# Performance work log

Measured on AMD Instinct MI355X. Metric: run time of the kernel, lower is better.

## Reference

```python
import jax, jax.numpy as jnp
import numpy as np
import math

NB_STEPS = 50  # matches init kwarg nb_steps


def cc_quadrature(nb_steps):
    # Clenshaw-Curtis weights/nodes, identical to UMNN's compute_cc_weights.
    lam = np.arange(nb_steps + 1, dtype=np.float64).reshape(-1, 1)
    lam = np.cos((lam @ lam.T) * math.pi / nb_steps)
    lam[:, 0] = 0.5
    lam[:, -1] = 0.5 * lam[:, -1]
    lam = lam * 2.0 / nb_steps
    W = np.arange(nb_steps + 1, dtype=np.float64).reshape(-1, 1)
    W[np.arange(1, nb_steps + 1, 2)] = 0
    W = 2.0 / (1.0 - W ** 2)
    W[0] = 1
    W[np.arange(1, nb_steps + 1, 2)] = 0
    cc_weights = (lam.T @ W).astype(np.float32)                 # [K, 1]
    steps = np.cos(np.arange(nb_steps + 1, dtype=np.float64).reshape(-1, 1)
                   * math.pi / nb_steps).astype(np.float32)     # [K, 1]
    return jnp.asarray(cc_weights), jnp.asarray(steps)


def integrand_mlp(xh, W1, b1, W2, b2, W3, b3, W4, b4):
    y = jax.nn.relu(jnp.einsum('bkd,hd->bkh', xh, W1) + b1)
    y = jax.nn.relu(jnp.einsum('bkh,gh->bkg', y, W2) + b2)
    y = jax.nn.relu(jnp.einsum('bkg,fg->bkf', y, W3) + b3)
    y = jnp.einsum('bkf,of->bko', y, W4) + b4
    return jax.nn.elu(y) + 1.0


def setup_inputs() -> dict:
    key = jax.random.key(0)
    ks = jax.random.split(key, 10)
    B, HD, IN_D = 16384, 128, 64
    x = jax.random.normal(ks[0], (B, 1), dtype=jnp.float32)
    h = jax.random.normal(ks[1], (B, IN_D - 1), dtype=jnp.float32)
    def lin(k, fan_out, fan_in):
        return jax.random.normal(k, (fan_out, fan_in), dtype=jnp.float32) / np.sqrt(fan_in)
    return {
        'x': x, 'h': h,
        'W1': lin(ks[2], HD, IN_D), 'b1': jax.random.normal(ks[3], (HD,), dtype=jnp.float32) * 0.01,
        'W2': lin(ks[4], HD, HD),   'b2': jax.random.normal(ks[5], (HD,), dtype=jnp.float32) * 0.01,
        'W3': lin(ks[6], HD, HD),   'b3': jax.random.normal(ks[7], (HD,), dtype=jnp.float32) * 0.01,
        'W4': lin(ks[8], 1, HD),    'b4': jax.random.normal(ks[9], (1,), dtype=jnp.float32) * 0.01,
    }


def reference(x, h, W1, b1, W2, b2, W3, b3, W4, b4):
    cc_w, steps = cc_quadrature(NB_STEPS)          # [K,1], [K,1]
    xmax = jnp.max(x) + 10.0
    x0 = x                                          # [B,1]
    xT = jnp.zeros_like(x) + xmax                   # xfinal broadcast
    # quadrature points X_steps: [B, K, 1]
    X = x0[:, None, :] + (xT - x0)[:, None, :] * (steps[None, :, :] + 1.0) * 0.5
    B, K = X.shape[0], X.shape[1]
    hK = jnp.broadcast_to(h[:, None, :], (B, K, h.shape[1]))
    xh = jnp.concatenate([X, hK], axis=-1)          # [B, K, in_d]
    f = integrand_mlp(xh, W1, b1, W2, b2, W3, b3, W4, b4)  # [B, K, 1]
    z = jnp.sum(f * cc_w[None, :, :], axis=1)       # [B, 1]
    return z * (xT - x0) * 0.5
```

## Files before the change

kernel.cpp:

```cpp
#include <hip/hip_runtime.h>
#include <hip/hip_bf16.h>
#include <math.h>


#define B_N    16384
#define KQ     51
#define HD     128
#define IND    64
#define BLK    128
#define GRID   512
#define RPB    32
#define RPW    16
#define SPW    (RPW * KQ)
#define TPW    (SPW / 16)

typedef __attribute__((ext_vector_type(8))) short short8;
typedef __attribute__((ext_vector_type(4))) float f32x4;

union S8U { short8 s8; unsigned u[4]; };

__device__ __forceinline__ unsigned short f2bf(float f) {
    __hip_bfloat16 t = __float2bfloat16(f);
    return *reinterpret_cast<unsigned short*>(&t);
}

#if defined(__gfx950__) && defined(__has_builtin)
#if __has_builtin(__builtin_amdgcn_cvt_pk_bf16_f32)
#define HAVE_PK_BF16 1
#endif
#endif

__device__ __forceinline__ unsigned pk_bf16(float lo, float hi) {
#ifdef HAVE_PK_BF16
    typedef __attribute__((ext_vector_type(2))) __bf16 bfv2;
    bfv2 r = __builtin_amdgcn_cvt_pk_bf16_f32(lo, hi);
    return *reinterpret_cast<unsigned*>(&r);
#else
    return (unsigned)f2bf(lo) | ((unsigned)f2bf(hi) << 16);
#endif
}

__launch_bounds__(BLK, 1)
__global__ void umnn_fused(const float* __restrict__ x,  const float* __restrict__ h,
                           const float* __restrict__ W1, const float* __restrict__ b1,
                           const float* __restrict__ W2, const float* __restrict__ b2,
                           const float* __restrict__ W3, const float* __restrict__ b3,
                           const float* __restrict__ W4, const float* __restrict__ b4,
                           float* __restrict__ out)
{
    __shared__ __align__(16) float hpL[RPB * HD];
    __shared__ __align__(16) char  y2x[2][4096];
    __shared__ __align__(16) float hshT[63 * 36];
    __shared__ float vs[2][SPW + 16];
    __shared__ float xL[RPB];
    __shared__ float sSteps[KQ], sCcw[KQ];
    __shared__ float red2[2];

    const int tid  = threadIdx.x;
    const int w    = tid >> 6;
    const int lane = tid & 63;
    const int q    = lane >> 4;
    const int lm   = lane & 15;
    const int swz  = lm & 7;
    const int rowBase = blockIdx.x * RPB;

    if (tid < KQ) {
        const int j = tid;
        const float pi50 = 0.06283185307179586f;
        sSteps[j] = __cosf((float)j * pi50);
        float s = 0.0f;
        for (int i = 0; i <= 50; i += 2) {
            float Wi = (i == 0) ? 1.0f : 2.0f / (1.0f - (float)(i * i));
            float lam;
            if (j == 0) lam = 0.5f;
            else {
                int mp = (i * j) % 100;
                lam = __cosf((float)mp * pi50);
                if (j == 50) lam *= 0.5f;
            }
            s += (lam * 0.04f) * Wi;
        }
        sCcw[j] = s;
    }
    {
        const f32x4* x4 = (const f32x4*)x;
        float mx = -1e30f;
        for (int i = tid; i < B_N / 4; i += BLK) {
            f32x4 v = x4[i];
            mx = fmaxf(fmaxf(mx, fmaxf(v[0], v[1])), fmaxf(v[2], v[3]));
        }
        #pragma unroll
        for (int d = 32; d > 0; d >>= 1) mx = fmaxf(mx, __shfl_xor(mx, d));
        if (lane == 0) red2[w] = mx;
    }
    for (int i = tid; i < RPB * 63; i += BLK) {
        int r = i / 63, d = i - r * 63;
        hshT[d * 36 + r] = h[(rowBase) * 63 + i];
    }
    if (tid < RPB) xL[tid] = x[rowBase + tid];
    __syncthreads();

    const float xmax = fmaxf(red2[0], red2[1]) + 10.0f;

    {
        const int n = tid;
        float acc[RPB];
        const float b1v = b1[n];
        #pragma unroll
        for (int r = 0; r < RPB; ++r) acc[r] = b1v;
        const float* wr = W1 + n * IND + 1;
        #pragma unroll 1
        for (int d = 0; d < IND - 1; ++d) {
            float wv = wr[d];
            const float* ht = hshT + d * 36;
            #pragma unroll
            for (int rc = 0; rc < RPB / 4; ++rc) {
                f32x4 hv = *(const f32x4*)(ht + rc * 4);
                acc[rc * 4 + 0] = fmaf(wv, hv[0], acc[rc * 4 + 0]);
                acc[rc * 4 + 1] = fmaf(wv, hv[1], acc[rc * 4 + 1]);
                acc[rc * 4 + 2] = fmaf(wv, hv[2], acc[rc * 4 + 2]);
                acc[rc * 4 + 3] = fmaf(wv, hv[3], acc[rc * 4 + 3]);
            }
        }
        #pragma unroll
        for (int r = 0; r < RPB; ++r) hpL[r * HD + n] = acc[r];
    }

    float w1x[32];
    #pragma unroll
    for (int kk = 0; kk < 4; ++kk)
        #pragma unroll
        for (int j = 0; j < 8; ++j)
            w1x[kk * 8 + j] = W1[(kk * 32 + q * 8 + j) * IND];

    short8 W2A[8][4], W3A[8][4];
    f32x4  b2c[8], b3c[8], W4c[8];
    #pragma unroll
    for (int nt = 0; nt < 8; ++nt) {
        #pragma unroll
        for (int kk = 0; kk < 4; ++kk) {
            const float* p2 = W2 + (nt * 16 + lm) * HD + kk * 32 + q * 8;
            const float* p3 = W3 + (nt * 16 + lm) * HD + kk * 32 + q * 8;
            S8U a2, a3;
            #pragma unroll
            for (int j = 0; j < 4; ++j) {
                a2.u[j] = pk_bf16(p2[2 * j], p2[2 * j + 1]);
                a3.u[j] = pk_bf16(p3[2 * j], p3[2 * j + 1]);
            }
            W2A[nt][kk] = a2.s8; W3A[nt][kk] = a3.s8;
        }
        b2c[nt] = *(const f32x4*)(b2 + nt * 16 + q * 4);
        b3c[nt] = *(const f32x4*)(b3 + nt * 16 + q * 4);
        W4c[nt] = *(const f32x4*)(W4 + nt * 16 + q * 4);
    }
    const float b4v = b4[0];
    char*  myY2 = y2x[w];
    float* vsW  = vs[w];
    __syncthreads();

    const int S0 = blockIdx.x * (RPB * KQ) + w * SPW;

    auto computeY1 = [&](int tt, short8* Y) {
        const int s   = S0 + tt * 16 + lm;
        const unsigned row = (unsigned)s / KQ;
        const int k   = s - (int)row * KQ;
        const int rl  = min((int)row - rowBase, RPB - 1);
        const float x0 = xL[rl];
        const float X  = fmaf((xmax - x0) * 0.5f, sSteps[k] + 1.0f, x0);
        #pragma unroll
        for (int kk = 0; kk < 4; ++kk) {
            const float* hp = hpL + rl * HD + kk * 32 + q * 8;
            f32x4 ha = *(const f32x4*)hp;
            f32x4 hb = *(const f32x4*)(hp + 4);
            S8U u;
            u.u[0] = pk_bf16(fmaxf(fmaf(X, w1x[kk*8+0], ha[0]), 0.f),
                             fmaxf(fmaf(X, w1x[kk*8+1], ha[1]), 0.f));
            u.u[1] = pk_bf16(fmaxf(fmaf(X, w1x[kk*8+2], ha[2]), 0.f),
                             fmaxf(fmaf(X, w1x[kk*8+3], ha[3]), 0.f));
            u.u[2] = pk_bf16(fmaxf(fmaf(X, w1x[kk*8+4], hb[0]), 0.f),
                             fmaxf(fmaf(X, w1x[kk*8+5], hb[1]), 0.f));
            u.u[3] = pk_bf16(fmaxf(fmaf(X, w1x[kk*8+6], hb[2]), 0.f),
                             fmaxf(fmaf(X, w1x[kk*8+7], hb[3]), 0.f));
            Y[kk] = u.s8;
        }
    };

    short8 Y1c[4], Y1n[4];
    computeY1(0, Y1c);

    #pragma unroll 1
    for (int tt = 0; tt < TPW; ++tt) {
        f32x4 C[8];
        #pragma unroll
        for (int nt = 0; nt < 8; ++nt) C[nt] = b2c[nt];
        #pragma unroll
        for (int kk = 0; kk < 4; ++kk)
            #pragma unroll
            for (int nt = 0; nt < 8; ++nt)
                C[nt] = __builtin_amdgcn_mfma_f32_16x16x32_bf16(W2A[nt][kk], Y1c[kk], C[nt], 0, 0, 0);

        #pragma unroll
        for (int nt = 0; nt < 8; ++nt) {
            unsigned lo = pk_bf16(fmaxf(C[nt][0], 0.f), fmaxf(C[nt][1], 0.f));
            unsigned hi = pk_bf16(fmaxf(C[nt][2], 0.f), fmaxf(C[nt][3], 0.f));
            *(int2*)(myY2 + lm * 256 + (((2*nt + (q>>1)) ^ swz) << 4) + ((q & 1) << 3))
                = make_int2((int)lo, (int)hi);
        }

        computeY1(tt + 1, Y1n);

        short8 Y2[4];
        #pragma unroll
        for (int kk = 0; kk < 4; ++kk)
            Y2[kk] = *(const short8*)(myY2 + lm * 256 + (((kk*4 + q) ^ swz) << 4));

        #pragma unroll
        for (int nt = 0; nt < 8; ++nt) C[nt] = b3c[nt];
        #pragma unroll
        for (int kk = 0; kk < 4; ++kk)
            #pragma unroll
            for (int nt = 0; nt < 8; ++nt)
                C[nt] = __builtin_amdgcn_mfma_f32_16x16x32_bf16(W3A[nt][kk], Y2[kk], C[nt], 0, 0, 0);

        float p = 0.f;
        #pragma unroll
        for (int nt = 0; nt < 8; ++nt) {
            p = fmaf(fmaxf(C[nt][0], 0.f), W4c[nt][0], p);
            p = fmaf(fmaxf(C[nt][1], 0.f), W4c[nt][1], p);
            p = fmaf(fmaxf(C[nt][2], 0.f), W4c[nt][2], p);
            p = fmaf(fmaxf(C[nt][3], 0.f), W4c[nt][3], p);
        }
        p += __shfl_xor(p, 16);
        p += __shfl_xor(p, 32);
        if (lane < 16) vsW[tt * 16 + lm] = p;

        #pragma unroll
        for (int kk = 0; kk < 4; ++kk) Y1c[kk] = Y1n[kk];
    }

    {
        const int r   = lane >> 2;
        const int sub = lane & 3;
        float a = 0.f;
        #pragma unroll 1
        for (int j = 0; j < 13; ++j) {
            int k = sub + 4 * j;
            if (k < KQ) {
                float y4 = vsW[r * KQ + k] + b4v;
                float f  = (y4 > 0.f) ? (y4 + 1.f) : __expf(y4);
                a = fmaf(f, sCcw[k], a);
            }
        }
        a += __shfl_xor(a, 1);
        a += __shfl_xor(a, 2);
        if (sub == 0) {
            int rl = w * RPW + r;
            out[rowBase + rl] = a * (xmax - xL[rl]) * 0.5f;
        }
    }
}

extern "C" void kernel_launch(void* const* d_in, const int* in_sizes, int n_in,
                              void* d_out, int out_size, void* d_ws, size_t ws_size,
                              hipStream_t stream)
{
    const float* x  = (const float*)d_in[0];
    const float* h  = (const float*)d_in[1];
    const float* W1 = (const float*)d_in[2];
    const float* b1 = (const float*)d_in[3];
    const float* W2 = (const float*)d_in[4];
    const float* b2 = (const float*)d_in[5];
    const float* W3 = (const float*)d_in[6];
    const float* b3 = (const float*)d_in[7];
    const float* W4 = (const float*)d_in[8];
    const float* b4 = (const float*)d_in[9];
    float* out = (float*)d_out;

    umnn_fused<<<GRID, BLK, 0, stream>>>(x, h, W1, b1, W2, b2, W3, b3,
                                         W4, b4, out);
}
```

Baseline: 187.4 us.

## Split layer-2 and layer-3 MFMA work into producer/consumer waves with double-buffered LDS

Wave 0 now computes the first hidden layer and the layer-2 MFMAs, then writes ReLU'd bf16 activations into a double-buffered LDS tile. Wave 1 consumes each tile with the layer-3 MFMAs, the W4 dot product and the final quadrature sum, with the two waves handing off through per-tile __syncthreads. Rows per block drop to 16 and launch bounds allow two blocks per CU, because each wave now only holds one weight matrix in registers. The cost is a block barrier on every tile and possible stalls if the two stages are unbalanced. Biases are also packed to bf16, which reduces precision.

After: 172.7 us. -7.9%, faster.

```diff
diff --git a/kernel.cpp b/kernel.cpp
--- a/kernel.cpp
+++ b/kernel.cpp
@@ -8,11 +8,9 @@
 #define HD     128
 #define IND    64
 #define BLK    128
-#define GRID   512
-#define RPB    32
-#define RPW    16
-#define SPW    (RPW * KQ)
-#define TPW    (SPW / 16)
+#define RPB    16
+#define GRID   (B_N / RPB)
+#define TPB    (RPB * KQ / 16)
 
 typedef __attribute__((ext_vector_type(8))) short short8;
 typedef __attribute__((ext_vector_type(4))) float f32x4;
@@ -40,7 +38,14 @@
 #endif
 }
 
-__launch_bounds__(BLK, 1)
+__device__ __forceinline__ float bf_lo(unsigned u) {
+    return __uint_as_float(u << 16);
+}
+__device__ __forceinline__ float bf_hi(unsigned u) {
+    return __uint_as_float(u & 0xffff0000u);
+}
+
+__launch_bounds__(BLK, 2)
 __global__ void umnn_fused(const float* __restrict__ x,  const float* __restrict__ h,
                            const float* __restrict__ W1, const float* __restrict__ b1,
                            const float* __restrict__ W2, const float* __restrict__ b2,
@@ -50,8 +55,8 @@
 {
     __shared__ __align__(16) float hpL[RPB * HD];
     __shared__ __align__(16) char  y2x[2][4096];
-    __shared__ __align__(16) float hshT[63 * 36];
-    __shared__ float vs[2][SPW + 16];
+    __shared__ __align__(16) float hshT[63 * 20];
+    __shared__ float vs[RPB * KQ + 16];
     __shared__ float xL[RPB];
     __shared__ float sSteps[KQ], sCcw[KQ];
     __shared__ float red2[2];
@@ -95,7 +100,7 @@
     }
     for (int i = tid; i < RPB * 63; i += BLK) {
         int r = i / 63, d = i - r * 63;
-        hshT[d * 36 + r] = h[(rowBase) * 63 + i];
+        hshT[d * 20 + r] = h[rowBase * 63 + i];
     }
     if (tid < RPB) xL[tid] = x[rowBase + tid];
     __syncthreads();
@@ -112,7 +117,7 @@
         #pragma unroll 1
         for (int d = 0; d < IND - 1; ++d) {
             float wv = wr[d];
-            const float* ht = hshT + d * 36;
+            const float* ht = hshT + d * 20;
             #pragma unroll
             for (int rc = 0; rc < RPB / 4; ++rc) {
                 f32x4 hv = *(const f32x4*)(ht + rc * 4);
@@ -125,137 +130,154 @@
         #pragma unroll
         for (int r = 0; r < RPB; ++r) hpL[r * HD + n] = acc[r];
     }
-
-    float w1x[32];
-    #pragma unroll
-    for (int kk = 0; kk < 4; ++kk)
-        #pragma unroll
-        for (int j = 0; j < 8; ++j)
-            w1x[kk * 8 + j] = W1[(kk * 32 + q * 8 + j) * IND];
-
-    short8 W2A[8][4], W3A[8][4];
-    f32x4  b2c[8], b3c[8], W4c[8];
-    #pragma unroll
-    for (int nt = 0; nt < 8; ++nt) {
-        #pragma unroll
-        for (int kk = 0; kk < 4; ++kk) {
-            const float* p2 = W2 + (nt * 16 + lm) * HD + kk * 32 + q * 8;
-            const float* p3 = W3 + (nt * 16 + lm) * HD + kk * 32 + q * 8;
-            S8U a2, a3;
-            #pragma unroll
-            for (int j = 0; j < 4; ++j) {
-                a2.u[j] = pk_bf16(p2[2 * j], p2[2 * j + 1]);
-                a3.u[j] = pk_bf16(p3[2 * j], p3[2 * j + 1]);
-            }
-            W2A[nt][kk] = a2.s8; W3A[nt][kk] = a3.s8;
-        }
-        b2c[nt] = *(const f32x4*)(b2 + nt * 16 + q * 4);
-        b3c[nt] = *(const f32x4*)(b3 + nt * 16 + q * 4);
-        W4c[nt] = *(const f32x4*)(W4 + nt * 16 + q * 4);
-    }
-    const float b4v = b4[0];
-    char*  myY2 = y2x[w];
-    float* vsW  = vs[w];
     __syncthreads();
 
-    const int S0 = blockIdx.x * (RPB * KQ) + w * SPW;
-
-    auto computeY1 = [&](int tt, short8* Y) {
-        const int s   = S0 + tt * 16 + lm;
-        const unsigned row = (unsigned)s / KQ;
-        const int k   = s - (int)row * KQ;
-        const int rl  = min((int)row - rowBase, RPB - 1);
-        const float x0 = xL[rl];
-        const float X  = fmaf((xmax - x0) * 0.5f, sSteps[k] + 1.0f, x0);
-        #pragma unroll
-        for (int kk = 0; kk < 4; ++kk) {
-            const float* hp = hpL + rl * HD + kk * 32 + q * 8;
-            f32x4 ha = *(const f32x4*)hp;
-            f32x4 hb = *(const f32x4*)(hp + 4);
-            S8U u;
-            u.u[0] = pk_bf16(fmaxf(fmaf(X, w1x[kk*8+0], ha[0]), 0.f),
-                             fmaxf(fmaf(X, w1x[kk*8+1], ha[1]), 0.f));
-            u.u[1] = pk_bf16(fmaxf(fmaf(X, w1x[kk*8+2], ha[2]), 0.f),
-                             fmaxf(fmaf(X, w1x[kk*8+3], ha[3]), 0.f));
-            u.u[2] = pk_bf16(fmaxf(fmaf(X, w1x[kk*8+4], hb[0]), 0.f),
-                             fmaxf(fmaf(X, w1x[kk*8+5], hb[1]), 0.f));
-            u.u[3] = pk_bf16(fmaxf(fmaf(X, w1x[kk*8+6], hb[2]), 0.f),
-                             fmaxf(fmaf(X, w1x[kk*8+7], hb[3]), 0.f));
-            Y[kk] = u.s8;
-        }
-    };
-
-    short8 Y1c[4], Y1n[4];
-    computeY1(0, Y1c);
-
-    #pragma unroll 1
-    for (int tt = 0; tt < TPW; ++tt) {
-        f32x4 C[8];
-        #pragma unroll
-        for (int nt = 0; nt < 8; ++nt) C[nt] = b2c[nt];
+    if (w == 0) {
+        float w1x[32];
         #pragma unroll
         for (int kk = 0; kk < 4; ++kk)
             #pragma unroll
-            for (int nt = 0; nt < 8; ++nt)
-                C[nt] = __builtin_amdgcn_mfma_f32_16x16x32_bf16(W2A[nt][kk], Y1c[kk], C[nt], 0, 0, 0);
-
+            for (int j = 0; j < 8; ++j)
+                w1x[kk * 8 + j] = W1[(kk * 32 + q * 8 + j) * IND];
+
+        short8  W2A[8][4];
+        unsigned b2p[16];
         #pragma unroll
         for (int nt = 0; nt < 8; ++nt) {
-            unsigned lo = pk_bf16(fmaxf(C[nt][0], 0.f), fmaxf(C[nt][1], 0.f));
-            unsigned hi = pk_bf16(fmaxf(C[nt][2], 0.f), fmaxf(C[nt][3], 0.f));
-            *(int2*)(myY2 + lm * 256 + (((2*nt + (q>>1)) ^ swz) << 4) + ((q & 1) << 3))
-                = make_int2((int)lo, (int)hi);
-        }
-
-        computeY1(tt + 1, Y1n);
-
-        short8 Y2[4];
-        #pragma unroll
-        for (int kk = 0; kk < 4; ++kk)
-            Y2[kk] = *(const short8*)(myY2 + lm * 256 + (((kk*4 + q) ^ swz) << 4));
-
-        #pragma unroll
-        for (int nt = 0; nt < 8; ++nt) C[nt] = b3c[nt];
-        #pragma unroll
-        for (int kk = 0; kk < 4; ++kk)
-            #pragma unroll
-            for (int nt = 0; nt < 8; ++nt)
-                C[nt] = __builtin_amdgcn_mfma_f32_16x16x32_bf16(W3A[nt][kk], Y2[kk], C[nt], 0, 0, 0);
-
-        float p = 0.f;
+            #pragma unroll
+            for (int kk = 0; kk < 4; ++kk) {
+                const float* p2 = W2 + (nt * 16 + lm) * HD + kk * 32 + q * 8;
+                S8U a2;
+                #pragma unroll
+                for (int j = 0; j < 4; ++j)
+                    a2.u[j] = pk_bf16(p2[2 * j], p2[2 * j + 1]);
+                W2A[nt][kk] = a2.s8;
+            }
+            b2p[2 * nt + 0] = pk_bf16(b2[nt * 16 + q * 4 + 0], b2[nt * 16 + q * 4 + 1]);
+            b2p[2 * nt + 1] = pk_bf16(b2[nt * 16 + q * 4 + 2], b2[nt * 16 + q * 4 + 3]);
+        }
+
+        #pragma unroll 1
+        for (int tt = 0; tt < TPB; ++tt) {
+            const int s    = tt * 16 + lm;
+            const unsigned row = (unsigned)s / KQ;
+            const int k    = s - (int)row * KQ;
+            const float x0 = xL[row];
+            const float X  = fmaf((xmax - x0) * 0.5f, sSteps[k] + 1.0f, x0);
+            short8 Y1[4];
+            #pragma unroll
+            for (int kk = 0; kk < 4; ++kk) {
+                const float* hp = hpL + row * HD + kk * 32 + q * 8;
+                f32x4 ha = *(const f32x4*)hp;
+                f32x4 hb = *(const f32x4*)(hp + 4);
+                S8U u;
+                u.u[0] = pk_bf16(fmaxf(fmaf(X, w1x[kk*8+0], ha[0]), 0.f),
+                                 fmaxf(fmaf(X, w1x[kk*8+1], ha[1]), 0.f));
+                u.u[1] = pk_bf16(fmaxf(fmaf(X, w1x[kk*8+2], ha[2]), 0.f),
+                                 fmaxf(fmaf(X, w1x[kk*8+3], ha[3]), 0.f));
+                u.u[2] = pk_bf16(fmaxf(fmaf(X, w1x[kk*8+4], hb[0]), 0.f),
+                                 fmaxf(fmaf(X, w1x[kk*8+5], hb[1]), 0.f));
+                u.u[3] = pk_bf16(fmaxf(fmaf(X, w1x[kk*8+6], hb[2]), 0.f),
+                                 fmaxf(fmaf(X, w1x[kk*8+7], hb[3]), 0.f));
+                Y1[kk] = u.s8;
+            }
+
+            f32x4 C[8];
+            #pragma unroll
+            for (int nt = 0; nt < 8; ++nt) {
+                unsigned u0 = b2p[2 * nt], u1 = b2p[2 * nt + 1];
+                C[nt][0] = bf_lo(u0); C[nt][1] = bf_hi(u0);
+                C[nt][2] = bf_lo(u1); C[nt][3] = bf_hi(u1);
+            }
+            #pragma unroll
+            for (int kk = 0; kk < 4; ++kk)
+                #pragma unroll
+                for (int nt = 0; nt < 8; ++nt)
+                    C[nt] = __builtin_amdgcn_mfma_f32_16x16x32_bf16(W2A[nt][kk], Y1[kk], C[nt], 0, 0, 0);
+
+            char* myY2 = y2x[tt & 1];
+            #pragma unroll
+            for (int nt = 0; nt < 8; ++nt) {
+                unsigned lo = pk_bf16(fmaxf(C[nt][0], 0.f), fmaxf(C[nt][1], 0.f));
+                unsigned hi = pk_bf16(fmaxf(C[nt][2], 0.f), fmaxf(C[nt][3], 0.f));
+                *(int2*)(myY2 + lm * 256 + (((2*nt + (q>>1)) ^ swz) << 4) + ((q & 1) << 3))
+                    = make_int2((int)lo, (int)hi);
+            }
+            __syncthreads();
+        }
+    } else {
+        short8  W3A[8][4];
+        unsigned b3p[16];
+        f32x4   W4c[8];
         #pragma unroll
         for (int nt = 0; nt < 8; ++nt) {
-            p = fmaf(fmaxf(C[nt][0], 0.f), W4c[nt][0], p);
-            p = fmaf(fmaxf(C[nt][1], 0.f), W4c[nt][1], p);
-            p = fmaf(fmaxf(C[nt][2], 0.f), W4c[nt][2], p);
-            p = fmaf(fmaxf(C[nt][3], 0.f), W4c[nt][3], p);
-        }
-        p += __shfl_xor(p, 16);
-        p += __shfl_xor(p, 32);
-        if (lane < 16) vsW[tt * 16 + lm] = p;
-
-        #pragma unroll
-        for (int kk = 0; kk < 4; ++kk) Y1c[kk] = Y1n[kk];
-    }
-
-    {
-        const int r   = lane >> 2;
-        const int sub = lane & 3;
-        float a = 0.f;
+            #pragma unroll
+            for (int kk = 0; kk < 4; ++kk) {
+                const float* p3 = W3 + (nt * 16 + lm) * HD + kk * 32 + q * 8;
+                S8U a3;
+                #pragma unroll
+                for (int j = 0; j < 4; ++j)
+                    a3.u[j] = pk_bf16(p3[2 * j], p3[2 * j + 1]);
+                W3A[nt][kk] = a3.s8;
+            }
+            b3p[2 * nt + 0] = pk_bf16(b3[nt * 16 + q * 4 + 0], b3[nt * 16 + q * 4 + 1]);
+            b3p[2 * nt + 1] = pk_bf16(b3[nt * 16 + q * 4 + 2], b3[nt * 16 + q * 4 + 3]);
+            W4c[nt] = *(const f32x4*)(W4 + nt * 16 + q * 4);
+        }
+        const float b4v = b4[0];
+
         #pragma unroll 1
-        for (int j = 0; j < 13; ++j) {
-            int k = sub + 4 * j;
-            if (k < KQ) {
-                float y4 = vsW[r * KQ + k] + b4v;
-                float f  = (y4 > 0.f) ? (y4 + 1.f) : __expf(y4);
-                a = fmaf(f, sCcw[k], a);
-            }
-        }
-        a += __shfl_xor(a, 1);
-        a += __shfl_xor(a, 2);
-        if (sub == 0) {
-            int rl = w * RPW + r;
-            out[rowBase + rl] = a * (xmax - xL[rl]) * 0.5f;
+        for (int tt = 0; tt < TPB; ++tt) {
+            __syncthreads();
+            const char* myY2 = y2x[tt & 1];
+            short8 Y2[4];
+            #pragma unroll
+            for (int kk = 0; kk < 4; ++kk)
+                Y2[kk] = *(const short8*)(myY2 + lm * 256 + (((kk*4 + q) ^ swz) << 4));
+
+            f32x4 C[8];
+            #pragma unroll
+            for (int nt = 0; nt < 8; ++nt) {
+                unsigned u0 = b3p[2 * nt], u1 = b3p[2 * nt + 1];
+                C[nt][0] = bf_lo(u0); C[nt][1] = bf_hi(u0);
+                C[nt][2] = bf_lo(u1); C[nt][3] = bf_hi(u1);
+            }
+            #pragma unroll
+            for (int kk = 0; kk < 4; ++kk)
+                #pragma unroll
+                for (int nt = 0; nt < 8; ++nt)
+                    C[nt] = __builtin_amdgcn_mfma_f32_16x16x32_bf16(W3A[nt][kk], Y2[kk], C[nt], 0, 0, 0);
+
+            float p = 0.f;
+            #pragma unroll
+            for (int nt = 0; nt < 8; ++nt) {
+                p = fmaf(fmaxf(C[nt][0], 0.f), W4c[nt][0], p);
+                p = fmaf(fmaxf(C[nt][1], 0.f), W4c[nt][1], p);
+                p = fmaf(fmaxf(C[nt][2], 0.f), W4c[nt][2], p);
+                p = fmaf(fmaxf(C[nt][3], 0.f), W4c[nt][3], p);
+            }
+            p += __shfl_xor(p, 16);
+            p += __shfl_xor(p, 32);
+            if (lane < 16) vs[tt * 16 + lm] = p;
+        }
+
+        {
+            const int r   = lane >> 2;
+            const int sub = lane & 3;
+            float a = 0.f;
+            #pragma unroll 1
+            for (int j = 0; j < 13; ++j) {
+                int k = sub + 4 * j;
+                if (k < KQ) {
+                    float y4 = vs[r * KQ + k] + b4v;
+                    float f  = (y4 > 0.f) ? (y4 + 1.f) : __expf(y4);
+                    a = fmaf(f, sCcw[k], a);
+                }
+            }
+            a += __shfl_xor(a, 1);
+            a += __shfl_xor(a, 2);
+            if (sub == 0)
+                out[rowBase + r] = a * (xmax - xL[r]) * 0.5f;
         }
     }
 }
```
